# Performance work log

Measured on AMD Instinct MI355X. Metric: run time of the kernel, lower is better.

## Reference

```python
import jax, jax.numpy as jnp
import numpy as np

H = 16  # num_heads
B, N, M, D = 4, 512, 2048, 1024
FF = 4096  # mlp_ratio * D
LN_EPS = 1e-5


def _ln(x, g, b):
    m = x.mean(-1, keepdims=True)
    v = ((x - m) ** 2).mean(-1, keepdims=True)
    return (x - m) * jax.lax.rsqrt(v + LN_EPS) * g + b


def _attn(q_in, k_in, v_in, wq, bq, wk, bk, wv, bv, wp, bp):
    b, n, d = q_in.shape
    m = k_in.shape[1]
    hd = d // H
    scale = hd ** -0.5
    q = (q_in @ wq + bq).reshape(b, n, H, hd) * scale
    k = (k_in @ wk + bk).reshape(b, m, H, hd)
    v = (v_in @ wv + bv).reshape(b, m, H, hd)
    attn = jax.nn.softmax(jnp.einsum('bnhd,bmhd->bhnm', q, k), axis=-1)
    out = jnp.einsum('bhnm,bmhd->bnhd', attn, v).reshape(b, n, d)
    return out @ wp + bp


def setup_inputs() -> dict:
    key = jax.random.key(0)
    ks = iter(jax.random.split(key, 32))
    rnd = lambda shape: jax.random.normal(next(ks), shape, dtype=jnp.float32)
    w = lambda *shape: rnd(shape) * 0.02
    inp = {
        'state': rnd((B, N, D)),
        'patches': rnd((B, M, D)),
        'patches_pos_embed': rnd((B, M, D)),
        'state_query': rnd((B, N, D)),
    }
    for p in ('ca', 'sa'):
        inp[f'{p}_wq'] = w(D, D); inp[f'{p}_bq'] = jnp.zeros((D,), jnp.float32)
        inp[f'{p}_wk'] = w(D, D); inp[f'{p}_bk'] = jnp.zeros((D,), jnp.float32)
        inp[f'{p}_wv'] = w(D, D); inp[f'{p}_bv'] = jnp.zeros((D,), jnp.float32)
        inp[f'{p}_wp'] = w(D, D); inp[f'{p}_bp'] = jnp.zeros((D,), jnp.float32)
    inp['w1'] = w(D, FF); inp['b1'] = jnp.zeros((FF,), jnp.float32)
    inp['w2'] = w(FF, D); inp['b2'] = jnp.zeros((D,), jnp.float32)
    for i in (1, 2, 3):
        inp[f'n{i}_g'] = jnp.ones((D,), jnp.float32)
        inp[f'n{i}_b'] = jnp.zeros((D,), jnp.float32)
        inp[f'ls{i}'] = jnp.full((D,), 1e-5, jnp.float32)
    return inp


def reference(state, patches, patches_pos_embed, state_query,
              ca_wq, ca_bq, ca_wk, ca_bk, ca_wv, ca_bv, ca_wp, ca_bp,
              sa_wq, sa_bq, sa_wk, sa_bk, sa_wv, sa_bv, sa_wp, sa_bp,
              w1, b1, w2, b2,
              n1_g, n1_b, n2_g, n2_b, n3_g, n3_b,
              ls1, ls2, ls3):
    # pre-norm path of TransformerLayer.forward_pre (dropouts/drop_path = 0)
    state = state + state_query
    kv = patches + patches_pos_embed
    cross = _attn(_ln(state, n1_g, n1_b), kv, patches,
                  ca_wq, ca_bq, ca_wk, ca_bk, ca_wv, ca_bv, ca_wp, ca_bp)
    state = state + cross * ls1
    ns = _ln(state, n2_g, n2_b)
    selfa = _attn(ns, ns, ns,
                  sa_wq, sa_bq, sa_wk, sa_bk, sa_wv, sa_bv, sa_wp, sa_bp)
    state = state + selfa * ls2
    h = jax.nn.gelu(_ln(state, n3_g, n3_b) @ w1 + b1)
    return state + (h @ w2 + b2) * ls3
```

## Files before the change

kernel.cpp:

```cpp
#include <hip/hip_runtime.h>

#define DEV __device__ __forceinline__

typedef __bf16 bf16x8 __attribute__((ext_vector_type(8)));
typedef float f32x4 __attribute__((ext_vector_type(4)));

DEV unsigned short f2bf(float f) {
  __bf16 h = (__bf16)f;
  return __builtin_bit_cast(unsigned short, h);
}
DEV unsigned int cvtpk(float lo, float hi) {
  unsigned int r;
  asm("v_cvt_pk_bf16_f32 %0, %1, %2" : "=v"(r) : "v"(lo), "v"(hi));
  return r;
}

DEV void gload16(const void* g, void* l) {
  __builtin_amdgcn_global_load_lds(
      (const __attribute__((address_space(1))) unsigned int*)g,
      (__attribute__((address_space(3))) unsigned int*)l, 16, 0, 0);
}

DEV float gelu(float v) {
  const float u = 0.7978845608028654f * (v + 0.044715f * v * v * v);
  const float e = exp2f(u * 2.885390081777927f);
  return 0.5f * v * (2.f - 2.f / (e + 1.f));
}

DEV void tconv64_body(const float* __restrict__ W, unsigned short* __restrict__ Wt,
                      int K, int N, int bx, int by, float* tile ) {
  const int t = threadIdx.x;
  const int rr = t >> 4;
  const int cc = (t & 15) * 4;
#pragma unroll
  for (int it = 0; it < 4; it++) {
    float4 v = *reinterpret_cast<const float4*>(
        &W[(size_t)(by * 64 + it * 16 + rr) * N + bx * 64 + cc]);
    tile[(it * 16 + rr) * 65 + cc] = v.x;
    tile[(it * 16 + rr) * 65 + cc + 1] = v.y;
    tile[(it * 16 + rr) * 65 + cc + 2] = v.z;
    tile[(it * 16 + rr) * 65 + cc + 3] = v.w;
  }
  __syncthreads();
  const int nr = t >> 3;
  const int kc = (t & 7) * 8;
#pragma unroll
  for (int it = 0; it < 2; it++) {
    const int n = it * 32 + nr;
    uint4 o;
    o.x = cvtpk(tile[(kc + 0) * 65 + n], tile[(kc + 1) * 65 + n]);
    o.y = cvtpk(tile[(kc + 2) * 65 + n], tile[(kc + 3) * 65 + n]);
    o.z = cvtpk(tile[(kc + 4) * 65 + n], tile[(kc + 5) * 65 + n]);
    o.w = cvtpk(tile[(kc + 6) * 65 + n], tile[(kc + 7) * 65 + n]);
    *reinterpret_cast<uint4*>(&Wt[(size_t)(bx * 64 + n) * K + by * 64 + kc]) = o;
  }
}

DEV void add_ln_body(const float* __restrict__ a, const float* b, float* x0_out,
                     unsigned short* __restrict__ y, const float* __restrict__ gam,
                     const float* __restrict__ bet, int row) {
  const int t = threadIdx.x;
  const int c = t * 4;
  const size_t base = (size_t)row * 1024 + c;
  float4 v = *reinterpret_cast<const float4*>(a + base);
  if (b) {
    float4 v2 = *reinterpret_cast<const float4*>(b + base);
    v.x += v2.x; v.y += v2.y; v.z += v2.z; v.w += v2.w;
  }
  if (x0_out) *reinterpret_cast<float4*>(x0_out + base) = v;
  float s = v.x + v.y + v.z + v.w;
  float sq = v.x * v.x + v.y * v.y + v.z * v.z + v.w * v.w;
#pragma unroll
  for (int o = 32; o > 0; o >>= 1) {
    s += __shfl_xor(s, o);
    sq += __shfl_xor(sq, o);
  }
  __shared__ float ps[4], pq[4];
  const int w = t >> 6;
  if ((t & 63) == 0) { ps[w] = s; pq[w] = sq; }
  __syncthreads();
  s = ps[0] + ps[1] + ps[2] + ps[3];
  sq = pq[0] + pq[1] + pq[2] + pq[3];
  const float mean = s * (1.f / 1024.f);
  const float var = sq * (1.f / 1024.f) - mean * mean;
  const float rstd = rsqrtf(var + 1e-5f);
  float4 gv = *reinterpret_cast<const float4*>(gam + c);
  float4 bv = *reinterpret_cast<const float4*>(bet + c);
  uint2 o2;
  o2.x = cvtpk((v.x - mean) * rstd * gv.x + bv.x, (v.y - mean) * rstd * gv.y + bv.y);
  o2.y = cvtpk((v.z - mean) * rstd * gv.z + bv.z, (v.w - mean) * rstd * gv.w + bv.w);
  *reinterpret_cast<uint2*>(y + base) = o2;
}

DEV void kvcast_body8(const float* __restrict__ p, const float* __restrict__ pe,
                      unsigned short* __restrict__ kvo, unsigned short* __restrict__ po,
                      int bid) {
  const size_t i = ((size_t)bid * 256 + threadIdx.x) * 8;
  float4 a0 = *reinterpret_cast<const float4*>(p + i);
  float4 a1 = *reinterpret_cast<const float4*>(p + i + 4);
  float4 b0 = *reinterpret_cast<const float4*>(pe + i);
  float4 b1 = *reinterpret_cast<const float4*>(pe + i + 4);
  uint4 kv, pp;
  kv.x = cvtpk(a0.x + b0.x, a0.y + b0.y);
  kv.y = cvtpk(a0.z + b0.z, a0.w + b0.w);
  kv.z = cvtpk(a1.x + b1.x, a1.y + b1.y);
  kv.w = cvtpk(a1.z + b1.z, a1.w + b1.w);
  pp.x = cvtpk(a0.x, a0.y);
  pp.y = cvtpk(a0.z, a0.w);
  pp.z = cvtpk(a1.x, a1.y);
  pp.w = cvtpk(a1.z, a1.w);
  *reinterpret_cast<uint4*>(kvo + i) = kv;
  *reinterpret_cast<uint4*>(po + i) = pp;
}

struct Pre {
  const float* caw[3]; unsigned short* cad[3];
  const float* state; const float* squery; float* stateF; unsigned short* lnB;
  const float* n1_g; const float* n1_b;
  const float* patches; const float* ppe; unsigned short* kvB; unsigned short* patB;
};
__global__ __launch_bounds__(256) void prelude_kernel(Pre p) {
  __shared__ __align__(16) float tile[64 * 65];
  const int bid = blockIdx.x;
  if (bid < 4096) {
    kvcast_body8(p.patches, p.ppe, p.kvB, p.patB, bid);
  } else if (bid < 4864) {
    const int i = bid - 4096;
    const int m = i >> 8, wi = i & 255;
    tconv64_body(p.caw[m], p.cad[m], 1024, 1024, wi & 15, wi >> 4, tile);
  } else {
    add_ln_body(p.state, p.squery, p.stateF, p.lnB, p.n1_g, p.n1_b, bid - 4864);
  }
}

__global__ __launch_bounds__(256) void add_ln_kernel(
    const float* __restrict__ a, const float* b, float* x0_out,
    unsigned short* __restrict__ y, const float* __restrict__ gam,
    const float* __restrict__ bet) {
  add_ln_body(a, b, x0_out, y, gam, bet, blockIdx.x);
}

DEV void xcd_swizzle(int gx, int gy, int& bx, int& by, int& bz) {
  const int gxy = gx * gy;
  const int nwg = gxy * gridDim.z;
  const int orig = (blockIdx.z * gy + blockIdx.y) * gx + blockIdx.x;
  const int q = nwg >> 3, r = nwg & 7;
  const int xcd = orig & 7;
  int wgid = (xcd < r ? xcd * (q + 1) : r * (q + 1) + (xcd - r) * q) + (orig >> 3);
  bz = wgid / gxy;
  wgid -= bz * gxy;
  if (gy >= gx) { by = wgid / gx; bx = wgid - by * gx; }
  else          { bx = wgid / gy; by = wgid - bx * gy; }
}

template <int BM, int BN>
DEV void gemm_core(const unsigned short* __restrict__ A,
                   const unsigned short* __restrict__ Bt,
                   unsigned short* As, unsigned short* Bs,
                   int brow, int bcol, int K, int lda, int koff,
                   f32x4 (&acc)[BM / 32][BN / 32]) {
  constexpr int WM = BM / 32, WN = BN / 32;
  const int t = threadIdx.x;
  const int lane = t & 63, w = t >> 6;
  const int wr = w >> 1, wc = w & 1;
  const int g = lane >> 4, lr = lane & 15;
  const int srow = lane >> 2, scol = (lane & 3) * 8;

  auto stage = [&](int buf, int k0) {
#pragma unroll
    for (int i = 0; i < BM / 64; i++) {
      const int r0 = (i * 4 + w) * 16;
      gload16(A + (size_t)(brow + r0 + srow) * lda + koff + k0 + scol,
              &As[buf * BM * 32 + r0 * 32]);
    }
#pragma unroll
    for (int i = 0; i < BN / 64; i++) {
      const int r0 = (i * 4 + w) * 16;
      gload16(Bt + (size_t)(bcol + r0 + srow) * lda + koff + k0 + scol,
              &Bs[buf * BN * 32 + r0 * 32]);
    }
  };

  stage(0, 0);
  const int nk = K / 32;
  int cur = 0;
  for (int kt = 0; kt < nk; kt++) {
    __syncthreads();
    if (kt + 1 < nk) stage(cur ^ 1, (kt + 1) * 32);
    bf16x8 af[WM], bfr[WN];
#pragma unroll
    for (int m = 0; m < WM; m++)
      af[m] = *reinterpret_cast<const bf16x8*>(
          &As[cur * BM * 32 + (wr * (BM / 2) + m * 16 + lr) * 32 + g * 8]);
#pragma unroll
    for (int n = 0; n < WN; n++)
      bfr[n] = *reinterpret_cast<const bf16x8*>(
          &Bs[cur * BN * 32 + (wc * (BN / 2) + n * 16 + lr) * 32 + g * 8]);
    __builtin_amdgcn_s_setprio(1);
#pragma unroll
    for (int m = 0; m < WM; m++)
#pragma unroll
      for (int n = 0; n < WN; n++)
        acc[m][n] = __builtin_amdgcn_mfma_f32_16x16x32_bf16(af[m], bfr[n], acc[m][n], 0, 0, 0);
    __builtin_amdgcn_s_setprio(0);
    cur ^= 1;
  }
}

template <int BM, int BN>
DEV void epilogue_vT(f32x4 (&acc)[BM / 32][BN / 32], unsigned short* smem,
                     unsigned short* __restrict__ vT, const float* __restrict__ bias,
                     int brow, int bcol, int vcol0, int vNk, int rpb) {
  constexpr int WM = BM / 32, WN = BN / 32;
  constexpr int LDT = 136;
  const int t = threadIdx.x, lane = t & 63, w = t >> 6;
  const int wr = w >> 1, wc = w & 1;
  const int g = lane >> 4, lr = lane & 15;
  __syncthreads();
#pragma unroll
  for (int m = 0; m < WM; m++) {
    const int row0 = wr * (BM / 2) + m * 16 + g * 4;
#pragma unroll
    for (int n = 0; n < WN; n++) {
      const int cc = wc * (BN / 2) + n * 16 + lr;
      const float bv = bias[bcol + cc];
      uint2 pk;
      pk.x = cvtpk(acc[m][n][0] + bv, acc[m][n][1] + bv);
      pk.y = cvtpk(acc[m][n][2] + bv, acc[m][n][3] + bv);
      *reinterpret_cast<uint2*>(&smem[cc * LDT + row0]) = pk;
    }
  }
  __syncthreads();
  const int b = brow / rpb;
  const int kvb = brow % rpb;
  constexpr int ITERS = BM * BN / (256 * 8);
#pragma unroll
  for (int it = 0; it < ITERS; it++) {
    const int idx = it * 256 + t;
    const int cc = idx / (BM / 8);
    const int ch = idx % (BM / 8);
    const int dg = bcol + cc - vcol0;
    const int h = dg >> 6, d = dg & 63;
    uint4 v = *reinterpret_cast<uint4*>(&smem[cc * LDT + ch * 8]);
    *reinterpret_cast<uint4*>(
        &vT[((size_t)(b * 16 + h) * 64 + d) * vNk + kvb + ch * 8]) = v;
  }
}

template <int EPI, int BM, int BN>
__global__ __launch_bounds__(256) void gemm_kernel(
    const unsigned short* __restrict__ A, const unsigned short* __restrict__ Bt,
    const float* __restrict__ bias, const float* resid,
    const float* __restrict__ ls, void* outp, int M, int N, int K, int lda) {
  constexpr int WM = BM / 32;
  constexpr int WN = BN / 32;
  __shared__ __align__(16) unsigned short smem[2 * BM * 32 + 2 * BN * 32];
  unsigned short* As = smem;
  unsigned short* Bs = smem + 2 * BM * 32;
  const int t = threadIdx.x;
  const int lane = t & 63, w = t >> 6;
  const int wr = w >> 1, wc = w & 1;
  const int g = lane >> 4, lr = lane & 15;

  int bx, by, bz;
  xcd_swizzle(gridDim.x, gridDim.y, bx, by, bz);
  const int brow = by * BM, bcol = bx * BN;

  f32x4 acc[WM][WN] = {};
  gemm_core<BM, BN>(A, Bt, As, Bs, brow, bcol, K, lda, bz * K, acc);

#pragma unroll
  for (int m = 0; m < WM; m++) {
    const int row0 = brow + wr * (BM / 2) + m * 16 + g * 4;
#pragma unroll
    for (int n = 0; n < WN; n++) {
      const int col = bcol + wc * (BN / 2) + n * 16 + lr;
      const float bv = (EPI == 4) ? 0.f : bias[col];
#pragma unroll
      for (int r = 0; r < 4; r++) {
        const float v = acc[m][n][r] + bv;
        const size_t idx = (size_t)(row0 + r) * N + col;
        if (EPI == 0) {
          ((unsigned short*)outp)[idx] = f2bf(v);
        } else if (EPI == 2) {
          ((float*)outp)[idx] = resid[idx] + v * ls[col];
        } else if (EPI == 3) {
          ((unsigned short*)outp)[idx] = f2bf(gelu(v));
        } else {
          ((float*)outp)[(size_t)bz * M * N + idx] = v;
        }
      }
    }
  }
}

struct G3X {
  const unsigned short* A[3]; const unsigned short* Bt[3];
  const float* bias[3]; unsigned short* out[3]; int ecum[3];
  unsigned short* vT; int vNk; int rpb;
  const float* wp; unsigned short* wpt;
  const float* saw[4]; unsigned short* sad[4];
  const float* bq; const float* bk; const float* bv; float* bqkv;
};
__global__ __launch_bounds__(256) void gemm3_kernel(G3X p, int N, int K) {
  constexpr int BM = 128, BN = 128, WM = BM / 32, WN = BN / 32;
  constexpr int STG = 2 * BM * 32 + 2 * BN * 32;
  constexpr int TRN = BN * 136;
  constexpr int SME = (TRN > STG) ? TRN : STG;
  constexpr int NG = 1152;
  __shared__ __align__(16) unsigned short smem[SME];
  const int bid = blockIdx.x;
  const int t = threadIdx.x;

  if (bid >= NG) {
    float* tile = reinterpret_cast<float*>(smem);
    int i = bid - NG;
    if (i < 256) {
      tconv64_body(p.wp, p.wpt, 1024, 1024, i & 15, i >> 4, tile);
    } else if (i < 1280) {
      i -= 256;
      const int m = i >> 8, wi = i & 255;
      tconv64_body(p.saw[m], p.sad[m], 1024, 1024, wi & 15, wi >> 4, tile);
    } else {
      const int j = (i - 1280) * 256 + t;
      p.bqkv[j] = j < 1024 ? p.bq[j] : (j < 2048 ? p.bk[j - 1024] : p.bv[j - 2048]);
    }
    return;
  }

  unsigned short* As = smem;
  unsigned short* Bs = smem + 2 * BM * 32;
  const int lane = t & 63, w = t >> 6;
  const int wr = w >> 1, wc = w & 1;
  const int g = lane >> 4, lr = lane & 15;
  const int wgid = (bid & 7) * (NG >> 3) + (bid >> 3);
  const int by = wgid >> 3, bx = wgid & 7;
  const int s = (by >= p.ecum[0]) + (by >= p.ecum[1]);
  const int byloc = by - (s ? p.ecum[s - 1] : 0);
  const unsigned short* A = p.A[s];
  const unsigned short* Bt = p.Bt[s];
  const float* bias = p.bias[s];
  const int brow = byloc * BM, bcol = bx * BN;

  f32x4 acc[WM][WN] = {};
  gemm_core<BM, BN>(A, Bt, As, Bs, brow, bcol, K, K, 0, acc);

  if (s == 2) {
    epilogue_vT<BM, BN>(acc, smem, p.vT, bias, brow, bcol, 0, p.vNk, p.rpb);
    return;
  }
  unsigned short* outp = p.out[s];
#pragma unroll
  for (int m = 0; m < WM; m++) {
    const int row0 = brow + wr * (BM / 2) + m * 16 + g * 4;
#pragma unroll
    for (int n = 0; n < WN; n++) {
      const int col = bcol + wc * (BN / 2) + n * 16 + lr;
      const float bv = bias[col];
#pragma unroll
      for (int r = 0; r < 4; r++)
        outp[(size_t)(row0 + r) * N + col] = f2bf(acc[m][n][r] + bv);
    }
  }
}

struct G5X {
  const unsigned short* A; const unsigned short* Bt;
  const float* bias; unsigned short* out;
  unsigned short* vT; int vcol0; int vNk; int rpb;
  const float* w1; unsigned short* w1t;
  const float* w2; unsigned short* w2t;
};
__global__ __launch_bounds__(256) void gemm5x_kernel(G5X p, int M, int N, int K) {
  constexpr int BM = 128, BN = 64, WM = BM / 32, WN = BN / 32;
  constexpr int STG = 2 * BM * 32 + 2 * BN * 32;
  __shared__ __align__(16) unsigned short smem[STG];
  constexpr int NG = 768;
  const int bid = blockIdx.x;
  const int t = threadIdx.x;

  if (bid >= NG) {
    float* tile = reinterpret_cast<float*>(smem);
    int i = bid - NG;
    if (i < 1024) {
      tconv64_body(p.w1, p.w1t, 1024, 4096, i & 63, i >> 6, tile);
    } else {
      i -= 1024;
      tconv64_body(p.w2, p.w2t, 4096, 1024, i & 15, i >> 4, tile);
    }
    return;
  }

  unsigned short* As = smem;
  unsigned short* Bs = smem + 2 * BM * 32;
  const int lane = t & 63, w = t >> 6;
  const int wr = w >> 1, wc = w & 1;
  const int g = lane >> 4, lr = lane & 15;
  const int wgid = (bid & 7) * (NG >> 3) + (bid >> 3);
  const int bx = wgid >> 4, by = wgid & 15;
  const int brow = by * BM, bcol = bx * BN;

  f32x4 acc[WM][WN] = {};
  gemm_core<BM, BN>(p.A, p.Bt, As, Bs, brow, bcol, K, K, 0, acc);

  if (bcol >= p.vcol0) {
    epilogue_vT<BM, BN>(acc, smem, p.vT, p.bias, brow, bcol, p.vcol0, p.vNk, p.rpb);
    return;
  }
#pragma unroll
  for (int m = 0; m < WM; m++) {
    const int row0 = brow + wr * (BM / 2) + m * 16 + g * 4;
#pragma unroll
    for (int n = 0; n < WN; n++) {
      const int col = bcol + wc * (BN / 2) + n * 16 + lr;
      const float bv = p.bias[col];
#pragma unroll
      for (int r = 0; r < 4; r++)
        p.out[(size_t)(row0 + r) * N + col] = f2bf(acc[m][n][r] + bv);
    }
  }
}

__global__ __launch_bounds__(256) void splitk_red_kernel(
    const float* __restrict__ p, const float* __restrict__ bias,
    const float* __restrict__ resid, const float* __restrict__ ls,
    float* __restrict__ out) {
  const size_t i = ((size_t)blockIdx.x * 256 + threadIdx.x) * 4;
  const int c = (int)(i & 1023);
  float4 a = *reinterpret_cast<const float4*>(p + i);
  float4 b = *reinterpret_cast<const float4*>(p + 2048ull * 1024 + i);
  float4 rv = *reinterpret_cast<const float4*>(resid + i);
  float4 bb = *reinterpret_cast<const float4*>(bias + c);
  float4 lv = *reinterpret_cast<const float4*>(ls + c);
  float4 o;
  o.x = rv.x + (a.x + b.x + bb.x) * lv.x;
  o.y = rv.y + (a.y + b.y + bb.y) * lv.y;
  o.z = rv.z + (a.z + b.z + bb.z) * lv.z;
  o.w = rv.w + (a.w + b.w + bb.w) * lv.w;
  *reinterpret_cast<float4*>(out + i) = o;
}

template <int SPLIT>
__global__ __launch_bounds__(512) void attn_kernel(
    const unsigned short* __restrict__ Q, const unsigned short* __restrict__ Kp,
    const unsigned short* __restrict__ vT, unsigned short* __restrict__ O,
    float* __restrict__ opart, float* __restrict__ mlbuf,
    int RSq, int RSk, int Nq, int NkTot, int NkL, float k2) {
  __shared__ __align__(16) unsigned short Ks[128 * 72];
  __shared__ __align__(16) unsigned short Vs[64 * 136];
  __shared__ __align__(16) unsigned short Ps[128 * 136];
  const int t = threadIdx.x, lane = t & 63, w = t >> 6;
  const int qt = blockIdx.y, h = blockIdx.x & 15, b = blockIdx.x >> 4;
  const int z = blockIdx.z;
  const int kvbase = z * NkL;
  const int g = lane >> 4, lr = lane & 15;
  const int ksrow = t >> 2, kscol = (t & 3) * 16;
  const int vsrow = t >> 3, vscol = (t & 7) * 16;

  uint4 qr[2];
  {
    const unsigned short* qp = Q + (size_t)(b * Nq + qt * 128 + w * 16 + lr) * RSq + h * 64 + g * 8;
    qr[0] = *reinterpret_cast<const uint4*>(qp);
    qr[1] = *reinterpret_cast<const uint4*>(qp + 32);
  }
  float m_i = -1e30f, l_i = 0.f;
  f32x4 acc_o[4] = {};

  auto kaddr = [&](int kv0) {
    return reinterpret_cast<const uint4*>(
        Kp + (size_t)(b * NkTot + kvbase + kv0 + ksrow) * RSk + h * 64 + kscol);
  };
  auto vaddr = [&](int kv0) {
    return reinterpret_cast<const uint4*>(
        vT + ((size_t)(b * 16 + h) * 64 + vsrow) * NkTot + kvbase + kv0 + vscol);
  };

  uint4 kr0 = kaddr(0)[0], kr1 = kaddr(0)[1];
  uint4 vr0 = vaddr(0)[0], vr1 = vaddr(0)[1];

  for (int kv0 = 0; kv0 < NkL; kv0 += 128) {
    *reinterpret_cast<uint4*>(&Ks[ksrow * 72 + kscol]) = kr0;
    *reinterpret_cast<uint4*>(&Ks[ksrow * 72 + kscol + 8]) = kr1;
    *reinterpret_cast<uint4*>(&Vs[vsrow * 136 + vscol]) = vr0;
    *reinterpret_cast<uint4*>(&Vs[vsrow * 136 + vscol + 8]) = vr1;
    __syncthreads();
    if (kv0 + 128 < NkL) {
      kr0 = kaddr(kv0 + 128)[0]; kr1 = kaddr(kv0 + 128)[1];
      vr0 = vaddr(kv0 + 128)[0]; vr1 = vaddr(kv0 + 128)[1];
    }

    f32x4 accs[8] = {};
    __builtin_amdgcn_s_setprio(1);
#pragma unroll
    for (int d0 = 0; d0 < 64; d0 += 32) {
      bf16x8 qf = __builtin_bit_cast(bf16x8, qr[d0 >> 5]);
#pragma unroll
      for (int m = 0; m < 8; m++) {
        bf16x8 kf = *reinterpret_cast<const bf16x8*>(&Ks[(m * 16 + lr) * 72 + d0 + g * 8]);
        accs[m] = __builtin_amdgcn_mfma_f32_16x16x32_bf16(kf, qf, accs[m], 0, 0, 0);
      }
    }
    __builtin_amdgcn_s_setprio(0);
    float pmax = -1e30f;
#pragma unroll
    for (int m = 0; m < 8; m++)
#pragma unroll
      for (int r = 0; r < 4; r++) pmax = fmaxf(pmax, accs[m][r]);
    pmax = fmaxf(pmax, __shfl_xor(pmax, 16));
    pmax = fmaxf(pmax, __shfl_xor(pmax, 32));
    const float pm2 = pmax * k2;
    if (!__all(pm2 <= m_i + 8.f)) {
      const float m_new = fmaxf(m_i, pm2);
      const float corr = exp2f(m_i - m_new);
      m_i = m_new;
      l_i *= corr;
#pragma unroll
      for (int r = 0; r < 4; r++) {
        const float cf = __shfl(corr, g * 4 + r);
#pragma unroll
        for (int n = 0; n < 4; n++) acc_o[n][r] *= cf;
      }
    }
    float psum = 0.f;
#pragma unroll
    for (int m = 0; m < 8; m++) {
      float p0 = exp2f(fmaf(accs[m][0], k2, -m_i));
      float p1 = exp2f(fmaf(accs[m][1], k2, -m_i));
      float p2 = exp2f(fmaf(accs[m][2], k2, -m_i));
      float p3 = exp2f(fmaf(accs[m][3], k2, -m_i));
      psum += p0 + p1 + p2 + p3;
      uint2 pk;
      pk.x = cvtpk(p0, p1);
      pk.y = cvtpk(p2, p3);
      *reinterpret_cast<uint2*>(&Ps[(w * 16 + lr) * 136 + m * 16 + g * 4]) = pk;
    }
    psum += __shfl_xor(psum, 16);
    psum += __shfl_xor(psum, 32);
    l_i += psum;
    __builtin_amdgcn_s_setprio(1);
#pragma unroll
    for (int ks = 0; ks < 4; ks++) {
      bf16x8 pf = *reinterpret_cast<const bf16x8*>(&Ps[(w * 16 + lr) * 136 + ks * 32 + g * 8]);
#pragma unroll
      for (int n = 0; n < 4; n++) {
        bf16x8 vf = *reinterpret_cast<const bf16x8*>(&Vs[(n * 16 + lr) * 136 + ks * 32 + g * 8]);
        acc_o[n] = __builtin_amdgcn_mfma_f32_16x16x32_bf16(pf, vf, acc_o[n], 0, 0, 0);
      }
    }
    __builtin_amdgcn_s_setprio(0);
    __syncthreads();
  }

  if (SPLIT) {
    const int R0 = ((b * 16 + h) << 9) + qt * 128 + w * 16;
    if (lane < 16) {
      mlbuf[(size_t)(R0 + lr) * 4 + z * 2] = m_i;
      mlbuf[(size_t)(R0 + lr) * 4 + z * 2 + 1] = l_i;
    }
#pragma unroll
    for (int r = 0; r < 4; r++) {
      const int R = R0 + g * 4 + r;
#pragma unroll
      for (int n = 0; n < 4; n++)
        opart[((size_t)z * 32768 + R) * 64 + n * 16 + lr] = acc_o[n][r];
    }
  } else {
#pragma unroll
    for (int r = 0; r < 4; r++) {
      const float li = __shfl(l_i, g * 4 + r);
      const float inv = 1.f / li;
      const int qrow = qt * 128 + w * 16 + g * 4 + r;
#pragma unroll
      for (int n = 0; n < 4; n++)
        O[(size_t)(b * Nq + qrow) * 1024 + h * 64 + n * 16 + lr] = f2bf(acc_o[n][r] * inv);
    }
  }
}

__global__ __launch_bounds__(256) void attn_combine_kernel(
    const float* __restrict__ opart, const float* __restrict__ mlbuf,
    unsigned short* __restrict__ O) {
  const int idx = blockIdx.x * 256 + threadIdx.x;
  const int R = idx >> 4;
  const int dq = (idx & 15) * 4;
  const float m1 = mlbuf[R * 4 + 0], l1 = mlbuf[R * 4 + 1];
  const float m2 = mlbuf[R * 4 + 2], l2 = mlbuf[R * 4 + 3];
  const float mm = fmaxf(m1, m2);
  const float e1 = exp2f(m1 - mm), e2 = exp2f(m2 - mm);
  const float inv = 1.f / (e1 * l1 + e2 * l2);
  float4 a = *reinterpret_cast<const float4*>(&opart[(size_t)R * 64 + dq]);
  float4 b = *reinterpret_cast<const float4*>(&opart[(size_t)(R + 32768) * 64 + dq]);
  const int bb = R >> 13, h = (R >> 9) & 15, q = R & 511;
  uint2 pk;
  pk.x = cvtpk((e1 * a.x + e2 * b.x) * inv, (e1 * a.y + e2 * b.y) * inv);
  pk.y = cvtpk((e1 * a.z + e2 * b.z) * inv, (e1 * a.w + e2 * b.w) * inv);
  *reinterpret_cast<uint2*>(O + ((size_t)(bb * 512 + q)) * 1024 + h * 64 + dq) = pk;
}

extern "C" void kernel_launch(void* const* d_in, const int* in_sizes, int n_in,
                              void* d_out, int out_size, void* d_ws, size_t ws_size,
                              hipStream_t stream) {
  const float* state = (const float*)d_in[0];
  const float* patches = (const float*)d_in[1];
  const float* ppe = (const float*)d_in[2];
  const float* squery = (const float*)d_in[3];
  const float* ca_wq = (const float*)d_in[4];
  const float* ca_bq = (const float*)d_in[5];
  const float* ca_wk = (const float*)d_in[6];
  const float* ca_bk = (const float*)d_in[7];
  const float* ca_wv = (const float*)d_in[8];
  const float* ca_bv = (const float*)d_in[9];
  const float* ca_wp = (const float*)d_in[10];
  const float* ca_bp = (const float*)d_in[11];
  const float* sa_wq = (const float*)d_in[12];
  const float* sa_bq = (const float*)d_in[13];
  const float* sa_wk = (const float*)d_in[14];
  const float* sa_bk = (const float*)d_in[15];
  const float* sa_wv = (const float*)d_in[16];
  const float* sa_bv = (const float*)d_in[17];
  const float* sa_wp = (const float*)d_in[18];
  const float* sa_bp = (const float*)d_in[19];
  const float* w1 = (const float*)d_in[20];
  const float* b1 = (const float*)d_in[21];
  const float* w2 = (const float*)d_in[22];
  const float* b2 = (const float*)d_in[23];
  const float* n1_g = (const float*)d_in[24];
  const float* n1_b = (const float*)d_in[25];
  const float* ls1 = (const float*)d_in[26];
  const float* n2_g = (const float*)d_in[27];
  const float* n2_b = (const float*)d_in[28];
  const float* ls2 = (const float*)d_in[29];
  const float* n3_g = (const float*)d_in[30];
  const float* n3_b = (const float*)d_in[31];
  const float* ls3 = (const float*)d_in[32];

  char* wsp = (char*)d_ws;
  auto alloc = [&](size_t bytes) {
    void* p = (void*)wsp;
    wsp += (bytes + 255) & ~(size_t)255;
    return p;
  };
  float* stateF = (float*)alloc(2048ull * 1024 * 4);
  unsigned short* lnB = (unsigned short*)alloc(2048ull * 1024 * 2);
  unsigned short* kvB = (unsigned short*)alloc(8192ull * 1024 * 2);
  unsigned short* patB = (unsigned short*)alloc(8192ull * 1024 * 2);
  unsigned short* qB = (unsigned short*)alloc(2048ull * 1024 * 2);
  unsigned short* kB = (unsigned short*)alloc(8192ull * 1024 * 2);
  unsigned short* vB = (unsigned short*)alloc(8192ull * 1024 * 2);
  unsigned short* oB = (unsigned short*)alloc(2048ull * 1024 * 2);
  unsigned short* hB = kvB;
  unsigned short* qkvB = kB;
  unsigned short* vTc = vB;
  unsigned short* vTs = qB;
  float* opart = (float*)patB;
  float* mlp2p = (float*)patB;
  unsigned short* ca_wqt = (unsigned short*)alloc(1024ull * 1024 * 2);
  unsigned short* ca_wkt = (unsigned short*)alloc(1024ull * 1024 * 2);
  unsigned short* ca_wvt = (unsigned short*)alloc(1024ull * 1024 * 2);
  unsigned short* ca_wpt = (unsigned short*)alloc(1024ull * 1024 * 2);
  unsigned short* sa_wqkvt = (unsigned short*)alloc(3072ull * 1024 * 2);
  unsigned short* sa_wpt = (unsigned short*)alloc(1024ull * 1024 * 2);
  unsigned short* w1t = (unsigned short*)alloc(4096ull * 1024 * 2);
  unsigned short* w2t = (unsigned short*)alloc(4096ull * 1024 * 2);
  float* sa_bqkv = (float*)alloc(3072 * 4);
  float* mlbuf = (float*)alloc(32768ull * 4 * 4);

  Pre pre;
  pre.caw[0] = ca_wq; pre.cad[0] = ca_wqt;
  pre.caw[1] = ca_wk; pre.cad[1] = ca_wkt;
  pre.caw[2] = ca_wv; pre.cad[2] = ca_wvt;
  pre.state = state; pre.squery = squery; pre.stateF = stateF; pre.lnB = lnB;
  pre.n1_g = n1_g; pre.n1_b = n1_b;
  pre.patches = patches; pre.ppe = ppe; pre.kvB = kvB; pre.patB = patB;
  prelude_kernel<<<6912, 256, 0, stream>>>(pre);

  const float k2 = 0.125f * 1.4426950408889634f;

  G3X g3;
  g3.A[0] = lnB;  g3.Bt[0] = ca_wqt; g3.bias[0] = ca_bq; g3.out[0] = qB;      g3.ecum[0] = 16;
  g3.A[1] = kvB;  g3.Bt[1] = ca_wkt; g3.bias[1] = ca_bk; g3.out[1] = kB;      g3.ecum[1] = 80;
  g3.A[2] = patB; g3.Bt[2] = ca_wvt; g3.bias[2] = ca_bv; g3.out[2] = nullptr; g3.ecum[2] = 144;
  g3.vT = vTc; g3.vNk = 2048; g3.rpb = 2048;
  g3.wp = ca_wp; g3.wpt = ca_wpt;
  g3.saw[0] = sa_wq; g3.sad[0] = sa_wqkvt;
  g3.saw[1] = sa_wk; g3.sad[1] = sa_wqkvt + 1024ull * 1024;
  g3.saw[2] = sa_wv; g3.sad[2] = sa_wqkvt + 2048ull * 1024;
  g3.saw[3] = sa_wp; g3.sad[3] = sa_wpt;
  g3.bq = sa_bq; g3.bk = sa_bk; g3.bv = sa_bv; g3.bqkv = sa_bqkv;
  gemm3_kernel<<<2444, 256, 0, stream>>>(g3, 1024, 1024);
  attn_kernel<1><<<dim3(64, 4, 2), 512, 0, stream>>>(
      qB, kB, vTc, nullptr, opart, mlbuf, 1024, 1024, 512, 2048, 1024, k2);
  attn_combine_kernel<<<2048, 256, 0, stream>>>(opart, mlbuf, oB);
  gemm_kernel<2, 64, 64><<<dim3(16, 32), 256, 0, stream>>>(oB, ca_wpt, ca_bp, stateF, ls1, stateF, 2048, 1024, 1024, 1024);

  add_ln_kernel<<<2048, 256, 0, stream>>>(stateF, nullptr, nullptr, lnB, n2_g, n2_b);
  G5X g5;
  g5.A = lnB; g5.Bt = sa_wqkvt; g5.bias = sa_bqkv; g5.out = qkvB;
  g5.vT = vTs; g5.vcol0 = 2048; g5.vNk = 512; g5.rpb = 512;
  g5.w1 = w1; g5.w1t = w1t; g5.w2 = w2; g5.w2t = w2t;
  gemm5x_kernel<<<2816, 256, 0, stream>>>(g5, 2048, 3072, 1024);
  attn_kernel<0><<<dim3(64, 4, 1), 512, 0, stream>>>(
      qkvB, qkvB + 1024, vTs, oB, nullptr, nullptr, 3072, 3072, 512, 512, 512, k2);
  gemm_kernel<2, 64, 64><<<dim3(16, 32), 256, 0, stream>>>(oB, sa_wpt, sa_bp, stateF, ls2, stateF, 2048, 1024, 1024, 1024);

  add_ln_kernel<<<2048, 256, 0, stream>>>(stateF, nullptr, nullptr, lnB, n3_g, n3_b);
  gemm_kernel<3, 128, 128><<<dim3(32, 16), 256, 0, stream>>>(lnB, w1t, b1, nullptr, nullptr, hB, 2048, 4096, 1024, 1024);
  gemm_kernel<4, 128, 64><<<dim3(16, 16, 2), 256, 0, stream>>>(hB, w2t, nullptr, nullptr, nullptr, mlp2p, 2048, 1024, 2048, 4096);
  splitk_red_kernel<<<2048, 256, 0, stream>>>(mlp2p, b2, stateF, ls3, (float*)d_out);
}
```

Before: 278.5 us.

## Replace cross-attn QKV GEMM with 256x256 tiled 8-wave pipelined kernel

Rewrites the fused cross-attention Q/K/V projection GEMM to use 256x256 tiles with 512 threads. It uses XOR-swizzled LDS staging via global_load_lds with double buffering, and interleaves four MFMA quadrant phases with staged loads, raw barriers and setprio. The weight-transpose side work is repacked so that each 512-thread block handles two 64x64 tiles. The aim is more data reuse per tile and better overlap of loads with MFMA, at the cost of heavy LDS use, fewer blocks (288 GEMM tiles), and fragile hand-written waitcnt/barrier ordering.

```diff
diff --git a/kernel.cpp b/kernel.cpp
--- a/kernel.cpp
+++ b/kernel.cpp
@@ -20,6 +20,10 @@
       (const __attribute__((address_space(1))) unsigned int*)g,
       (__attribute__((address_space(3))) unsigned int*)l, 16, 0, 0);
 }
+
+template <int N>
+DEV void vmw() { asm volatile("s_waitcnt vmcnt(%0)" :: "i"(N) : "memory"); }
+DEV void barx() { asm volatile("s_barrier" ::: "memory"); }
 
 DEV float gelu(float v) {
   const float u = 0.7978845608028654f * (v + 0.044715f * v * v * v);
@@ -44,6 +48,34 @@
   __syncthreads();
   const int nr = t >> 3;
   const int kc = (t & 7) * 8;
+#pragma unroll
+  for (int it = 0; it < 2; it++) {
+    const int n = it * 32 + nr;
+    uint4 o;
+    o.x = cvtpk(tile[(kc + 0) * 65 + n], tile[(kc + 1) * 65 + n]);
+    o.y = cvtpk(tile[(kc + 2) * 65 + n], tile[(kc + 3) * 65 + n]);
+    o.z = cvtpk(tile[(kc + 4) * 65 + n], tile[(kc + 5) * 65 + n]);
+    o.w = cvtpk(tile[(kc + 6) * 65 + n], tile[(kc + 7) * 65 + n]);
+    *reinterpret_cast<uint4*>(&Wt[(size_t)(bx * 64 + n) * K + by * 64 + kc]) = o;
+  }
+}
+
+DEV void tconv64_pair(const float* __restrict__ W, unsigned short* __restrict__ Wt,
+                      int K, int N, int bx, int by, float* tile, int tid) {
+  const int rr = tid >> 4;
+  const int cc = (tid & 15) * 4;
+#pragma unroll
+  for (int it = 0; it < 4; it++) {
+    float4 v = *reinterpret_cast<const float4*>(
+        &W[(size_t)(by * 64 + it * 16 + rr) * N + bx * 64 + cc]);
+    tile[(it * 16 + rr) * 65 + cc] = v.x;
+    tile[(it * 16 + rr) * 65 + cc + 1] = v.y;
+    tile[(it * 16 + rr) * 65 + cc + 2] = v.z;
+    tile[(it * 16 + rr) * 65 + cc + 3] = v.w;
+  }
+  __syncthreads();
+  const int nr = tid >> 3;
+  const int kc = (tid & 7) * 8;
 #pragma unroll
   for (int it = 0; it < 2; it++) {
     const int n = it * 32 + nr;
@@ -294,7 +326,21 @@
   }
 }
 
-struct G3X {
+template <int QM, int QN>
+DEV void mm_phase(f32x4 (&acc)[8][4], const bf16x8 (&a)[4][2], const bf16x8 (&b)[2][2]) {
+  __builtin_amdgcn_s_setprio(1);
+#pragma unroll
+  for (int mi = 0; mi < 4; mi++)
+#pragma unroll
+    for (int ni = 0; ni < 2; ni++)
+#pragma unroll
+      for (int kk = 0; kk < 2; kk++)
+        acc[QM * 4 + mi][QN * 2 + ni] = __builtin_amdgcn_mfma_f32_16x16x32_bf16(
+            a[mi][kk], b[ni][kk], acc[QM * 4 + mi][QN * 2 + ni], 0, 0, 0);
+  __builtin_amdgcn_s_setprio(0);
+}
+
+struct G8P {
   const unsigned short* A[3]; const unsigned short* Bt[3];
   const float* bias[3]; unsigned short* out[3]; int ecum[3];
   unsigned short* vT; int vNk; int rpb;
@@ -302,60 +348,159 @@
   const float* saw[4]; unsigned short* sad[4];
   const float* bq; const float* bk; const float* bv; float* bqkv;
 };
-__global__ __launch_bounds__(256) void gemm3_kernel(G3X p, int N, int K) {
-  constexpr int BM = 128, BN = 128, WM = BM / 32, WN = BN / 32;
-  constexpr int STG = 2 * BM * 32 + 2 * BN * 32;
-  constexpr int TRN = BN * 136;
-  constexpr int SME = (TRN > STG) ? TRN : STG;
-  constexpr int NG = 1152;
-  __shared__ __align__(16) unsigned short smem[SME];
+__global__ __launch_bounds__(512, 2) void gemm8p_kernel(G8P p, int N, int K) {
+  constexpr int NG = 288;
+  __shared__ __align__(16) unsigned short smem[65536];
   const int bid = blockIdx.x;
   const int t = threadIdx.x;
 
   if (bid >= NG) {
-    float* tile = reinterpret_cast<float*>(smem);
     int i = bid - NG;
-    if (i < 256) {
-      tconv64_body(p.wp, p.wpt, 1024, 1024, i & 15, i >> 4, tile);
-    } else if (i < 1280) {
-      i -= 256;
-      const int m = i >> 8, wi = i & 255;
-      tconv64_body(p.saw[m], p.sad[m], 1024, 1024, wi & 15, wi >> 4, tile);
+    const int tid = t & 255, sel = t >> 8;
+    float* tile = reinterpret_cast<float*>(smem) + sel * 4224;
+    if (i < 128) {
+      const int ti = i * 2 + sel;
+      tconv64_pair(p.wp, p.wpt, 1024, 1024, ti & 15, ti >> 4, tile, tid);
+    } else if (i < 640) {
+      const int ti = (i - 128) * 2 + sel;
+      const int m = ti >> 8, wi = ti & 255;
+      tconv64_pair(p.saw[m], p.sad[m], 1024, 1024, wi & 15, wi >> 4, tile, tid);
     } else {
-      const int j = (i - 1280) * 256 + t;
-      p.bqkv[j] = j < 1024 ? p.bq[j] : (j < 2048 ? p.bk[j - 1024] : p.bv[j - 2048]);
+      const int j = (i - 640) * 512 + t;
+      if (j < 3072)
+        p.bqkv[j] = j < 1024 ? p.bq[j] : (j < 2048 ? p.bk[j - 1024] : p.bv[j - 2048]);
     }
     return;
   }
 
-  unsigned short* As = smem;
-  unsigned short* Bs = smem + 2 * BM * 32;
-  const int lane = t & 63, w = t >> 6;
-  const int wr = w >> 1, wc = w & 1;
-  const int g = lane >> 4, lr = lane & 15;
-  const int wgid = (bid & 7) * (NG >> 3) + (bid >> 3);
-  const int by = wgid >> 3, bx = wgid & 7;
+  const int wgid = (bid & 7) * 36 + (bid >> 3);
+  const int bx = wgid & 3, by = wgid >> 2;
   const int s = (by >= p.ecum[0]) + (by >= p.ecum[1]);
   const int byloc = by - (s ? p.ecum[s - 1] : 0);
   const unsigned short* A = p.A[s];
   const unsigned short* Bt = p.Bt[s];
   const float* bias = p.bias[s];
-  const int brow = byloc * BM, bcol = bx * BN;
-
-  f32x4 acc[WM][WN] = {};
-  gemm_core<BM, BN>(A, Bt, As, Bs, brow, bcol, K, K, 0, acc);
+  const int brow = byloc * 256, bcol = bx * 256;
+
+  unsigned short* AsL = smem;
+  unsigned short* BsL = smem + 32768;
+
+  const int w = t >> 6, lane = t & 63;
+  const int wr = w >> 2, wc = w & 3;
+  const int g = lane >> 4, lr = lane & 15;
+  const int sr8 = t >> 3;
+  const int scx = (((t & 7) ^ ((t >> 3) & 7)) << 3);
+  const int wvb = w << 3;
+
+  auto stageA = [&](int buf, int T, int h) {
+#pragma unroll
+    for (int i = 0; i < 2; i++)
+      gload16(A + (size_t)(brow + h * 128 + i * 64 + sr8) * K + T * 64 + scx,
+              &AsL[buf * 16384 + (h * 128 + i * 64 + wvb) * 64]);
+  };
+  auto stageB = [&](int buf, int T, int h) {
+#pragma unroll
+    for (int i = 0; i < 2; i++)
+      gload16(Bt + (size_t)(bcol + h * 128 + i * 64 + sr8) * K + T * 64 + scx,
+              &BsL[buf * 16384 + (h * 128 + i * 64 + wvb) * 64]);
+  };
+
+  bf16x8 a[4][2], b0[2][2], b1[2][2];
+  auto loadA = [&](int buf, int qm) {
+#pragma unroll
+    for (int mi = 0; mi < 4; mi++) {
+      const int row = qm * 128 + wr * 64 + mi * 16 + lr;
+#pragma unroll
+      for (int kk = 0; kk < 2; kk++)
+        a[mi][kk] = *reinterpret_cast<const bf16x8*>(
+            &AsL[buf * 16384 + row * 64 + ((((kk << 2) + g) ^ (row & 7)) << 3)]);
+    }
+  };
+  auto loadB = [&](int buf, int qn, bf16x8 (&b)[2][2]) {
+#pragma unroll
+    for (int ni = 0; ni < 2; ni++) {
+      const int row = qn * 128 + wc * 32 + ni * 16 + lr;
+#pragma unroll
+      for (int kk = 0; kk < 2; kk++)
+        b[ni][kk] = *reinterpret_cast<const bf16x8*>(
+            &BsL[buf * 16384 + row * 64 + ((((kk << 2) + g) ^ (row & 7)) << 3)]);
+    }
+  };
+
+  f32x4 acc[8][4] = {};
+
+  stageA(0, 0, 0); stageB(0, 0, 0); stageA(0, 0, 1); stageB(0, 0, 1);
+  stageA(1, 1, 0); stageB(1, 1, 1);
+  vmw<4>();
+  barx();
+
+  const int nk = K >> 6;
+  for (int T = 0; T < nk; T++) {
+    const int buf = T & 1;
+    loadA(buf, 0); loadB(buf, 0, b0);
+    if (T + 1 < nk) stageB(buf ^ 1, T + 1, 0);
+    barx();
+    mm_phase<0, 0>(acc, a, b0);
+    barx();
+    loadB(buf, 1, b1);
+    if (T + 1 < nk) stageA(buf ^ 1, T + 1, 1);
+    barx();
+    mm_phase<0, 1>(acc, a, b1);
+    barx();
+    loadA(buf, 1);
+    if (T + 2 < nk) stageA(buf, T + 2, 0);
+    barx();
+    mm_phase<1, 1>(acc, a, b1);
+    barx();
+    if (T + 2 < nk) { stageB(buf, T + 2, 1); vmw<4>(); } else { vmw<0>(); }
+    barx();
+    mm_phase<1, 0>(acc, a, b0);
+    barx();
+  }
+  vmw<0>();
+  barx();
 
   if (s == 2) {
-    epilogue_vT<BM, BN>(acc, smem, p.vT, bias, brow, bcol, 0, p.vNk, p.rpb);
+    const int b_ = brow / p.rpb;
+    const int kvb = brow % p.rpb;
+#pragma unroll
+    for (int h2 = 0; h2 < 2; h2++) {
+      if (h2) barx();
+#pragma unroll
+      for (int mi = 0; mi < 4; mi++) {
+        const int m = h2 * 4 + mi;
+        const int rowL = wr * 64 + mi * 16 + g * 4;
+#pragma unroll
+        for (int n = 0; n < 4; n++) {
+          const int cc = (n >> 1) * 128 + wc * 32 + (n & 1) * 16 + lr;
+          const float bv = bias[bcol + cc];
+          uint2 pk;
+          pk.x = cvtpk(acc[m][n][0] + bv, acc[m][n][1] + bv);
+          pk.y = cvtpk(acc[m][n][2] + bv, acc[m][n][3] + bv);
+          *reinterpret_cast<uint2*>(&smem[cc * 136 + rowL]) = pk;
+        }
+      }
+      barx();
+#pragma unroll
+      for (int it = 0; it < 8; it++) {
+        const int idx = it * 512 + t;
+        const int cc = idx >> 4, ch = idx & 15;
+        const int dg = bcol + cc;
+        const int hh = dg >> 6, dd = dg & 63;
+        uint4 v = *reinterpret_cast<uint4*>(&smem[cc * 136 + ch * 8]);
+        *reinterpret_cast<uint4*>(
+            &p.vT[((size_t)(b_ * 16 + hh) * 64 + dd) * p.vNk + kvb + h2 * 128 + ch * 8]) = v;
+      }
+    }
     return;
   }
   unsigned short* outp = p.out[s];
 #pragma unroll
-  for (int m = 0; m < WM; m++) {
-    const int row0 = brow + wr * (BM / 2) + m * 16 + g * 4;
-#pragma unroll
-    for (int n = 0; n < WN; n++) {
-      const int col = bcol + wc * (BN / 2) + n * 16 + lr;
+  for (int m = 0; m < 8; m++) {
+    const int row0 = brow + (m >> 2) * 128 + wr * 64 + (m & 3) * 16 + g * 4;
+#pragma unroll
+    for (int n = 0; n < 4; n++) {
+      const int col = bcol + (n >> 1) * 128 + wc * 32 + (n & 1) * 16 + lr;
       const float bv = bias[col];
 #pragma unroll
       for (int r = 0; r < 4; r++)
@@ -676,18 +821,18 @@
 
   const float k2 = 0.125f * 1.4426950408889634f;
 
-  G3X g3;
-  g3.A[0] = lnB;  g3.Bt[0] = ca_wqt; g3.bias[0] = ca_bq; g3.out[0] = qB;      g3.ecum[0] = 16;
-  g3.A[1] = kvB;  g3.Bt[1] = ca_wkt; g3.bias[1] = ca_bk; g3.out[1] = kB;      g3.ecum[1] = 80;
-  g3.A[2] = patB; g3.Bt[2] = ca_wvt; g3.bias[2] = ca_bv; g3.out[2] = nullptr; g3.ecum[2] = 144;
-  g3.vT = vTc; g3.vNk = 2048; g3.rpb = 2048;
-  g3.wp = ca_wp; g3.wpt = ca_wpt;
-  g3.saw[0] = sa_wq; g3.sad[0] = sa_wqkvt;
-  g3.saw[1] = sa_wk; g3.sad[1] = sa_wqkvt + 1024ull * 1024;
-  g3.saw[2] = sa_wv; g3.sad[2] = sa_wqkvt + 2048ull * 1024;
-  g3.saw[3] = sa_wp; g3.sad[3] = sa_wpt;
-  g3.bq = sa_bq; g3.bk = sa_bk; g3.bv = sa_bv; g3.bqkv = sa_bqkv;
-  gemm3_kernel<<<2444, 256, 0, stream>>>(g3, 1024, 1024);
+  G8P g8;
+  g8.A[0] = lnB;  g8.Bt[0] = ca_wqt; g8.bias[0] = ca_bq; g8.out[0] = qB;      g8.ecum[0] = 8;
+  g8.A[1] = kvB;  g8.Bt[1] = ca_wkt; g8.bias[1] = ca_bk; g8.out[1] = kB;      g8.ecum[1] = 40;
+  g8.A[2] = patB; g8.Bt[2] = ca_wvt; g8.bias[2] = ca_bv; g8.out[2] = nullptr; g8.ecum[2] = 72;
+  g8.vT = vTc; g8.vNk = 2048; g8.rpb = 2048;
+  g8.wp = ca_wp; g8.wpt = ca_wpt;
+  g8.saw[0] = sa_wq; g8.sad[0] = sa_wqkvt;
+  g8.saw[1] = sa_wk; g8.sad[1] = sa_wqkvt + 1024ull * 1024;
+  g8.saw[2] = sa_wv; g8.sad[2] = sa_wqkvt + 2048ull * 1024;
+  g8.saw[3] = sa_wp; g8.sad[3] = sa_wpt;
+  g8.bq = sa_bq; g8.bk = sa_bk; g8.bv = sa_bv; g8.bqkv = sa_bqkv;
+  gemm8p_kernel<<<934, 512, 0, stream>>>(g8, 1024, 1024);
   attn_kernel<1><<<dim3(64, 4, 2), 512, 0, stream>>>(
       qB, kB, vTc, nullptr, opart, mlbuf, 1024, 1024, 512, 2048, 1024, k2);
   attn_combine_kernel<<<2048, 256, 0, stream>>>(opart, mlbuf, oB);
```

Result: no change. 282.4 us (+1.4%).
